# Kernel optimization log

Measured on AMD Instinct MI355X. Metric: run time of the kernel, lower is better.

The kernel has to match this reference:

```python
import jax, jax.numpy as jnp
import numpy as np

BLOCK_SIZE = 64
NUM_STEPS = 3
# pad_type='post', init_type='ones', attention_mask=None


def setup_inputs() -> dict:
    key = jax.random.key(0)
    k1, k2, k3 = jax.random.split(key, 3)
    B, H, S, D = 4, 16, 4096, 64
    return {
        "query": jax.random.normal(k1, (B, H, S, D), dtype=jnp.float32),
        "key": jax.random.normal(k2, (B, H, S, D), dtype=jnp.float32),
        "value": jax.random.normal(k3, (B, H, S, D), dtype=jnp.float32),
    }


def _soba_monarch(query, key, value):
    B, H, S, D = query.shape
    bs = BLOCK_SIZE
    nb = -(-S // bs)                 # ceil(S / bs)
    pad = nb * bs - S                # post padding amount
    q = query / (D ** 0.5)

    pad_cfg = ((0, 0), (0, 0), (0, pad), (0, 0))
    Qb = jnp.pad(q, pad_cfg).reshape(B, H, nb, bs, D)      # (l j) v -> l j v
    Kb = jnp.pad(key, pad_cfg).reshape(B, H, nb, bs, D)    # (k i) v -> k i v

    # validity of positions in the padded sequence (post-pad)
    pos_valid = (jnp.arange(nb * bs) < S).reshape(nb, bs)  # [block, within]
    # left factor shape (..., j, l, k): rows of the flattened (l j) axis
    left_mask = jnp.broadcast_to(pos_valid.T[:, :, None], (bs, nb, nb))      # j l k
    # right factor shape (..., k, j, i): columns of the flattened (k i) axis
    right_mask = jnp.broadcast_to(pos_valid[:, None, :], (nb, bs, bs))       # k j i

    NEG = jnp.finfo(q.dtype).min
    # init_type = 'ones'
    left = jnp.broadcast_to(
        jnp.where(left_mask, 1.0 / nb, 0.0), (B, H, bs, nb, nb)
    ).astype(q.dtype)

    for _ in range(NUM_STEPS):
        # beta[k,j,i] = sum_{l,v} left[j,l,k] Q[l,j,v] K[k,i,v]
        beta = jnp.einsum('bhjlk,bhljv,bhkiv->bhkji', left, Qb, Kb, optimize=True)
        tau = jnp.swapaxes(jnp.sum(left, axis=-2), -1, -2)[..., None]        # bhkj1
        tau_zero = jnp.isclose(tau, 0.0)
        tau_safe = jnp.where(tau_zero, 1.0, tau)
        logits_r = jnp.where(right_mask & ~tau_zero, beta / tau_safe, NEG)
        right = jax.nn.softmax(logits_r, axis=-1)
        right = jnp.where(right_mask, right, 0.0)

        # alpha[j,1,k] = sum_i right[k,j,i] log right[k,j,i]  (xlogy)
        r_safe = jnp.where(right > 0, right, 1.0)
        alpha = jnp.sum(right * jnp.log(r_safe), axis=-1)                    # bhkj
        alpha = jnp.swapaxes(alpha, -1, -2)[..., None, :]                    # bhj1k

        beta2 = jnp.einsum('bhkji,bhljv,bhkiv->bhjlk', right, Qb, Kb, optimize=True)
        left = jax.nn.softmax(jnp.where(left_mask, beta2 - alpha, NEG), axis=-1)
        left = jnp.where(left_mask, left, 0.0)

    # multiply: z = L (R V)
    Vb = jnp.pad(value, pad_cfg).reshape(B, H, nb, bs, D)                    # k i v
    Y = jnp.einsum('bhkji,bhkiv->bhkjv', right, Vb)
    Z = jnp.einsum('bhjlk,bhkjv->bhljv', left, Y)
    z = Z.reshape(B, H, nb * bs, D)
    return z[..., :S, :]


def reference(query, key, value):
    return _soba_monarch(query, key, value)
```

## Files before the change

kernel.cpp:

```cpp
#include <hip/hip_runtime.h>


namespace {

typedef __attribute__((ext_vector_type(8))) short short8v;
typedef __attribute__((ext_vector_type(4))) float f32x4;

constexpr int HEADS = 64;
constexpr size_t HEADQ = 262144;
constexpr size_t MATF  = (size_t)HEADS * 262144;

#define MFMA(ACC, A, B) ACC = __builtin_amdgcn_mfma_f32_16x16x32_bf16(A, B, ACC, 0, 0, 0)
#define LD8(arr, row, g8) (*(const short8v*)((arr) + (row) * 72 + (g8) * 8))

__device__ __forceinline__ void bfsplit(float x, ushort& h, ushort& l) {
    uint u = __float_as_uint(x);
    uint hi = (u + 0x7FFFu + ((u >> 16) & 1u)) & 0xFFFF0000u;
    h = (ushort)(hi >> 16);
    l = (ushort)(__float_as_uint(x - __uint_as_float(hi)) >> 16);
}
__device__ __forceinline__ uint packbf(float x) {
    uint u = __float_as_uint(x);
    uint hi = (u + 0x7FFFu + ((u >> 16) & 1u)) & 0xFFFF0000u;
    return hi | (__float_as_uint(x - __uint_as_float(hi)) >> 16);
}

struct Frag16 { short8v h0, h1, l0, l1; };

__device__ __forceinline__ Frag16 split_load(const float* __restrict__ p, float s) {
    Frag16 f;
    #pragma unroll
    for (int q = 0; q < 4; ++q) {
        float4 a = *(const float4*)(p + 4 * q);
        float v[4] = {a.x * s, a.y * s, a.z * s, a.w * s};
        #pragma unroll
        for (int e = 0; e < 4; ++e) {
            ushort hh, ll; bfsplit(v[e], hh, ll);
            const int i = 4 * q + e;
            if (i < 8) { f.h0[i] = (short)hh; f.l0[i] = (short)ll; }
            else       { f.h1[i - 8] = (short)hh; f.l1[i - 8] = (short)ll; }
        }
    }
    return f;
}
__device__ __forceinline__ Frag16 unpack_load(const uint* __restrict__ p) {
    Frag16 f;
    #pragma unroll
    for (int q = 0; q < 2; ++q) {
        uint4 a = *(const uint4*)(p + 8 * q);
        uint4 b = *(const uint4*)(p + 8 * q + 4);
        uint vv[8] = {a.x, a.y, a.z, a.w, b.x, b.y, b.z, b.w};
        short8v h, l;
        #pragma unroll
        for (int e = 0; e < 8; ++e) {
            h[e] = (short)(vv[e] >> 16);
            l[e] = (short)(vv[e] & 0xFFFFu);
        }
        if (q == 0) { f.h0 = h; f.l0 = l; } else { f.h1 = h; f.l1 = l; }
    }
    return f;
}
__device__ __forceinline__ void store_rows(ushort* H, ushort* L, int r, int c0,
                                           const Frag16& f) {
    *(short8v*)(H + r * 72 + c0)     = f.h0;
    *(short8v*)(H + r * 72 + c0 + 8) = f.h1;
    *(short8v*)(L + r * 72 + c0)     = f.l0;
    *(short8v*)(L + r * 72 + c0 + 8) = f.l1;
}
__device__ __forceinline__ void scatter_tr(ushort* H, ushort* L, int r, int c0,
                                           const Frag16& f) {
    #pragma unroll
    for (int e = 0; e < 8; ++e) {
        H[(c0 + e) * 72 + r] = (ushort)f.h0[e];
        L[(c0 + e) * 72 + r] = (ushort)f.l0[e];
    }
    #pragma unroll
    for (int e = 0; e < 8; ++e) {
        H[(c0 + 8 + e) * 72 + r] = (ushort)f.h1[e];
        L[(c0 + 8 + e) * 72 + r] = (ushort)f.l1[e];
    }
}

__device__ __forceinline__ void mmstep(const ushort* AH, const ushort* AL,
                                       const ushort* BH, const ushort* BL,
                                       int w, int lo4, int hi4, f32x4 acc[4]) {
    #pragma unroll
    for (int ks = 0; ks < 2; ++ks) {
        short8v ah = LD8(AH, 16 * w + lo4, hi4 + 4 * ks);
        short8v al = LD8(AL, 16 * w + lo4, hi4 + 4 * ks);
        #pragma unroll
        for (int t = 0; t < 4; ++t) {
            short8v bh = LD8(BH, 16 * t + lo4, hi4 + 4 * ks);
            short8v bl = LD8(BL, 16 * t + lo4, hi4 + 4 * ks);
            MFMA(acc[t], ah, bh); MFMA(acc[t], ah, bl); MFMA(acc[t], al, bh);
        }
    }
}
__device__ __forceinline__ void mmstep_swap(const ushort* AH, const ushort* AL,
                                            const ushort* BH, const ushort* BL,
                                            int w, int lo4, int hi4, f32x4 acc[4]) {
    #pragma unroll
    for (int ks = 0; ks < 2; ++ks) {
        short8v bh = LD8(AH, 16 * w + lo4, hi4 + 4 * ks);
        short8v bl = LD8(AL, 16 * w + lo4, hi4 + 4 * ks);
        #pragma unroll
        for (int m = 0; m < 4; ++m) {
            short8v ah = LD8(BH, 16 * m + lo4, hi4 + 4 * ks);
            short8v al = LD8(BL, 16 * m + lo4, hi4 + 4 * ks);
            MFMA(acc[m], ah, bh); MFMA(acc[m], ah, bl); MFMA(acc[m], al, bh);
        }
    }
}

__device__ __forceinline__ float max16(const float* x) {
    float a = fmaxf(fmaxf(x[0], x[1]), fmaxf(x[2], x[3]));
    float b = fmaxf(fmaxf(x[4], x[5]), fmaxf(x[6], x[7]));
    float c = fmaxf(fmaxf(x[8], x[9]), fmaxf(x[10], x[11]));
    float d = fmaxf(fmaxf(x[12], x[13]), fmaxf(x[14], x[15]));
    return fmaxf(fmaxf(a, b), fmaxf(c, d));
}
__device__ __forceinline__ float sum16(const float* x) {
    float a = (x[0] + x[1]) + (x[2] + x[3]);
    float b = (x[4] + x[5]) + (x[6] + x[7]);
    float c = (x[8] + x[9]) + (x[10] + x[11]);
    float d = (x[12] + x[13]) + (x[14] + x[15]);
    return (a + b) + (c + d);
}

__global__ __launch_bounds__(256) void kmean_kernel(const float* __restrict__ Q,
                                                    uint* __restrict__ M) {
    const int wg = blockIdx.x;
    const int h  = wg >> 4;
    const int j  = ((wg & 15) << 2) + (threadIdx.x >> 6);
    const int v  = threadIdx.x & 63;
    const float* base = Q + (size_t)h * HEADQ + (size_t)j * 64 + v;
    float acc = 0.f;
    #pragma unroll
    for (int l = 0; l < 64; ++l) acc += base[(size_t)l * 4096];
    M[((size_t)h * 64 + j) * 64 + v] = packbf(acc * (1.0f / 512.0f));
}

template<int FIRST, int LAST>
__global__ __launch_bounds__(256, 4) void bc_kernel(
    const uint*  __restrict__ Gsrc,
    const float* __restrict__ Kmat,
    const float* __restrict__ Vmat,
    const float* __restrict__ tauIn,
    uint*  __restrict__ HmOut,
    float* __restrict__ alphaOut,
    uint*  __restrict__ Yout)
{
    __shared__ __align__(16) ushort SM[18432];
    ushort* Ah = SM;          ushort* Al = SM + 4608;
    ushort* Bh = SM + 9216;   ushort* Bl = SM + 13824;

    const int wg = blockIdx.x, h = wg >> 6, k = wg & 63;
    const int tid = threadIdx.x, r = tid & 63, c0 = (tid >> 6) << 4;
    const int w = tid >> 6, lo4 = tid & 15, hi4 = (tid >> 4) & 3;

    {
        const uint* gp = FIRST ? Gsrc + ((size_t)h * 64 + r) * 64 + c0
                               : Gsrc + ((size_t)h * 64 + r) * 4096 + (size_t)k * 64 + c0;
        store_rows(Ah, Al, r, c0, unpack_load(gp));
    }
    Frag16 fk = split_load(Kmat + (size_t)h * HEADQ + (size_t)k * 4096 + r * 64 + c0, 1.f);
    store_rows(Bh, Bl, r, c0, fk);
    Frag16 fv;
    if (LAST)
        fv = split_load(Vmat + (size_t)h * HEADQ + (size_t)k * 4096 + r * 64 + c0, 1.f);
    float tv = 1.f;
    if (!FIRST) tv = tauIn[((size_t)h * 64 + k) * 64 + 16 * w + lo4];
    __syncthreads();

    f32x4 acc[4] = {};
    mmstep_swap(Ah, Al, Bh, Bl, w, lo4, hi4, acc);
    __syncthreads();

    {
        const int j = 16 * w + lo4;
        const bool tz = !(tv > 1e-8f);
        const float tvi = tz ? 1.f : 1.f / tv;
        float x[16];
        #pragma unroll
        for (int m = 0; m < 4; ++m)
            #pragma unroll
            for (int rg = 0; rg < 4; ++rg) x[4 * m + rg] = acc[m][rg] * tvi;
        float mx = max16(x);
        mx = fmaxf(mx, __shfl_xor(mx, 16));
        mx = fmaxf(mx, __shfl_xor(mx, 32));
        #pragma unroll
        for (int e = 0; e < 16; ++e) x[e] = __expf(x[e] - mx);
        float s = sum16(x);
        s += __shfl_xor(s, 16);
        s += __shfl_xor(s, 32);
        const float inv = 1.f / s;
        float ap = 0.f;
        #pragma unroll
        for (int m = 0; m < 4; ++m) {
            #pragma unroll
            for (int rg = 0; rg < 4; ++rg) {
                const float rv = tz ? (1.f / 64.f) : x[4 * m + rg] * inv;
                ap += (rv > 0.f) ? rv * __logf(rv) : 0.f;
                ushort hh, ll; bfsplit(rv, hh, ll);
                const int i = 16 * m + 4 * hi4 + rg;
                Ah[j * 72 + i] = hh;
                Al[j * 72 + i] = ll;
            }
        }
        ap += __shfl_xor(ap, 16);
        ap += __shfl_xor(ap, 32);
        if (hi4 == 0) alphaOut[((size_t)h * 64 + j) * 64 + k] = ap;
    }
    scatter_tr(Bh, Bl, r, c0, fk);
    __syncthreads();

    f32x4 acc2[4] = {};
    mmstep(Ah, Al, Bh, Bl, w, lo4, hi4, acc2);
    #pragma unroll
    for (int rr = 0; rr < 4; ++rr) {
        const int j = 16 * w + 4 * hi4 + rr;
        const size_t ob = ((size_t)h * 64 + k) * 4096 + (size_t)j * 64;
        #pragma unroll
        for (int t = 0; t < 4; ++t)
            HmOut[ob + 16 * t + lo4] = packbf(acc2[t][rr]);
    }
    if (LAST) {
        __syncthreads();
        scatter_tr(Bh, Bl, r, c0, fv);
        __syncthreads();
        f32x4 acc3[4] = {};
        mmstep(Ah, Al, Bh, Bl, w, lo4, hi4, acc3);
        #pragma unroll
        for (int rr = 0; rr < 4; ++rr) {
            const int j = 16 * w + 4 * hi4 + rr;
            const size_t ob = ((size_t)h * 64 + k) * 4096 + (size_t)j * 64;
            #pragma unroll
            for (int t = 0; t < 4; ++t)
                Yout[ob + 16 * t + lo4] = packbf(acc3[t][rr]);
        }
    }
}

template<int LAST>
__global__ __launch_bounds__(256, 4) void da_kernel(
    const float* __restrict__ Q,
    const uint*  __restrict__ HmIn,
    const float* __restrict__ alphaIn,
    const uint*  __restrict__ Yin,
    uint*  __restrict__ Gout,
    float* __restrict__ tauOut,
    float* __restrict__ Zout)
{
    __shared__ __align__(16) ushort SM[18432];
    ushort* Ah = SM;          ushort* Al = SM + 4608;
    ushort* Bh = SM + 9216;   ushort* Bl = SM + 13824;

    const int wg = blockIdx.x, h = wg >> 6, j = wg & 63;
    const int tid = threadIdx.x, r = tid & 63, c0 = (tid >> 6) << 4;
    const int w = tid >> 6, lo4 = tid & 15, hi4 = (tid >> 4) & 3;

    Frag16 fq = split_load(Q + (size_t)h * HEADQ + (size_t)r * 4096 + (size_t)j * 64 + c0,
                           0.125f);
    store_rows(Ah, Al, r, c0, fq);
    {
        store_rows(Bh, Bl, r, c0,
                   unpack_load(HmIn + ((size_t)h * 64 + r) * 4096 + (size_t)j * 64 + c0));
    }
    Frag16 fy;
    if (LAST)
        fy = unpack_load(Yin + ((size_t)h * 64 + r) * 4096 + (size_t)j * 64 + c0);
    float av[16];
    {
        const float* ap0 = alphaIn + ((size_t)h * 64 + j) * 64 + 4 * hi4;
        #pragma unroll
        for (int m = 0; m < 4; ++m)
            #pragma unroll
            for (int rg = 0; rg < 4; ++rg) av[4 * m + rg] = ap0[16 * m + rg];
    }
    __syncthreads();

    f32x4 acc[4] = {};
    mmstep_swap(Ah, Al, Bh, Bl, w, lo4, hi4, acc);
    __syncthreads();

    {
        const int l = 16 * w + lo4;
        float x[16];
        #pragma unroll
        for (int m = 0; m < 4; ++m)
            #pragma unroll
            for (int rg = 0; rg < 4; ++rg) x[4 * m + rg] = acc[m][rg] - av[4 * m + rg];
        float mx = max16(x);
        mx = fmaxf(mx, __shfl_xor(mx, 16));
        mx = fmaxf(mx, __shfl_xor(mx, 32));
        #pragma unroll
        for (int e = 0; e < 16; ++e) x[e] = __expf(x[e] - mx);
        float s = sum16(x);
        s += __shfl_xor(s, 16);
        s += __shfl_xor(s, 32);
        const float inv = 1.f / s;
        #pragma unroll
        for (int m = 0; m < 4; ++m) {
            #pragma unroll
            for (int rg = 0; rg < 4; ++rg) {
                const float lv = x[4 * m + rg] * inv;
                ushort hh, ll; bfsplit(lv, hh, ll);
                const int kk = 16 * m + 4 * hi4 + rg;
                if (!LAST) { Bh[kk * 72 + l] = hh; Bl[kk * 72 + l] = ll; }
                else       { Bh[l * 72 + kk] = hh; Bl[l * 72 + kk] = ll; }
            }
        }
    }
    if (!LAST) scatter_tr(Ah, Al, r, c0, fq);
    else       scatter_tr(Ah, Al, r, c0, fy);
    __syncthreads();

    if (!LAST) {
        f32x4 acc2[4] = {};
        f32x4 tacc = {};
        short8v onesb;
        #pragma unroll
        for (int e2 = 0; e2 < 8; ++e2) onesb[e2] = (lo4 == 0) ? (short)0x3F80 : (short)0;
        #pragma unroll
        for (int ks = 0; ks < 2; ++ks) {
            short8v ah = LD8(Bh, 16 * w + lo4, hi4 + 4 * ks);
            short8v al = LD8(Bl, 16 * w + lo4, hi4 + 4 * ks);
            MFMA(tacc, ah, onesb); MFMA(tacc, al, onesb);
            #pragma unroll
            for (int t = 0; t < 4; ++t) {
                short8v bh = LD8(Ah, 16 * t + lo4, hi4 + 4 * ks);
                short8v bl = LD8(Al, 16 * t + lo4, hi4 + 4 * ks);
                MFMA(acc2[t], ah, bh); MFMA(acc2[t], ah, bl); MFMA(acc2[t], al, bh);
            }
        }
        #pragma unroll
        for (int rr = 0; rr < 4; ++rr) {
            const int kq = 16 * w + 4 * hi4 + rr;
            if (lo4 == 0) tauOut[((size_t)h * 64 + kq) * 64 + j] = tacc[rr];
            const size_t gb = ((size_t)h * 64 + j) * 4096 + (size_t)kq * 64;
            #pragma unroll
            for (int t = 0; t < 4; ++t) Gout[gb + 16 * t + lo4] = packbf(acc2[t][rr]);
        }
    } else {
        f32x4 acc2[4] = {};
        #pragma unroll
        for (int ks = 0; ks < 2; ++ks) {
            short8v ah = LD8(Bh, 16 * w + lo4, hi4 + 4 * ks);
            short8v al = LD8(Bl, 16 * w + lo4, hi4 + 4 * ks);
            #pragma unroll
            for (int t = 0; t < 4; ++t) {
                short8v bh = LD8(Ah, 16 * t + lo4, hi4 + 4 * ks);
                short8v bl = LD8(Al, 16 * t + lo4, hi4 + 4 * ks);
                MFMA(acc2[t], ah, bh); MFMA(acc2[t], ah, bl); MFMA(acc2[t], al, bh);
            }
        }
        #pragma unroll
        for (int rr = 0; rr < 4; ++rr) {
            const int l = 16 * w + 4 * hi4 + rr;
            const size_t zb = (size_t)h * HEADQ + (size_t)l * 4096 + (size_t)j * 64;
            #pragma unroll
            for (int t = 0; t < 4; ++t) Zout[zb + 16 * t + lo4] = acc2[t][rr];
        }
    }
}

}

extern "C" void kernel_launch(void* const* d_in, const int* in_sizes, int n_in,
                              void* d_out, int out_size, void* d_ws, size_t ws_size,
                              hipStream_t stream) {
    const float* Q = (const float*)d_in[0];
    const float* K = (const float*)d_in[1];
    const float* V = (const float*)d_in[2];
    float* out = (float*)d_out;

    char* ws = (char*)d_ws;
    const size_t MB = 1024 * 1024;
    uint*  G   = (uint*)(ws);
    uint*  Hm  = (uint*)(ws + 64 * MB);
    uint*  M   = (uint*)(ws + 128 * MB);
    float* al  = (float*)(ws + 129 * MB);
    float* tau = (float*)(ws + 130 * MB);

    const bool bigws = ws_size >= (size_t)195 * MB;
    uint*  Ybuf = bigws ? (uint*)(ws + 131 * MB) : (uint*)out;
    float* Zdst = bigws ? out : (float*)G;

    dim3 blk(256), grid(HEADS * 64);

    kmean_kernel<<<dim3(1024), blk, 0, stream>>>(Q, M);
    bc_kernel<1, 0><<<grid, blk, 0, stream>>>(M, K, nullptr, nullptr, Hm, al, nullptr);
    da_kernel<0>   <<<grid, blk, 0, stream>>>(Q, Hm, al, nullptr, G, tau, nullptr);
    bc_kernel<0, 0><<<grid, blk, 0, stream>>>(G, K, nullptr, tau, Hm, al, nullptr);
    da_kernel<0>   <<<grid, blk, 0, stream>>>(Q, Hm, al, nullptr, G, tau, nullptr);
    bc_kernel<0, 1><<<grid, blk, 0, stream>>>(G, K, V, tau, Hm, al, Ybuf);
    da_kernel<1>   <<<grid, blk, 0, stream>>>(Q, Hm, al, Ybuf, nullptr, nullptr, Zdst);
    if (!bigws)
        hipMemcpyAsync(d_out, Zdst, MATF * sizeof(float), hipMemcpyDeviceToDevice, stream);
}
```

Baseline: 310.6 us.

## Stage outputs through LDS for coalesced stores, swizzle workgroups, transpose tau/alpha layout

Output tiles (Hm, Y, G, Z) are first written to a padded LDS buffer and then flushed with 128-bit coalesced global stores, replacing scattered 4-byte stores. Workgroup IDs are remapped with an 8-way swizzle, which changes which blocks run close together and so may affect cache locality. The tau and alpha index layouts are transposed so their reads and writes follow the access pattern of the consuming kernel. The bf16 hi/lo split now uses the library conversion intrinsic. The LDS staging adds extra barriers and LDS traffic.

```diff
diff --git a/kernel.cpp b/kernel.cpp
--- a/kernel.cpp
+++ b/kernel.cpp
@@ -1,4 +1,5 @@
 #include <hip/hip_runtime.h>
+#include <hip/hip_bf16.h>
 
 
 namespace {
@@ -13,16 +14,19 @@
 #define MFMA(ACC, A, B) ACC = __builtin_amdgcn_mfma_f32_16x16x32_bf16(A, B, ACC, 0, 0, 0)
 #define LD8(arr, row, g8) (*(const short8v*)((arr) + (row) * 72 + (g8) * 8))
 
+__device__ __forceinline__ ushort bfh(float x) {
+    return __builtin_bit_cast(ushort, __float2bfloat16(x));
+}
+__device__ __forceinline__ float bf2f(ushort h) {
+    return __uint_as_float(((uint)h) << 16);
+}
 __device__ __forceinline__ void bfsplit(float x, ushort& h, ushort& l) {
-    uint u = __float_as_uint(x);
-    uint hi = (u + 0x7FFFu + ((u >> 16) & 1u)) & 0xFFFF0000u;
-    h = (ushort)(hi >> 16);
-    l = (ushort)(__float_as_uint(x - __uint_as_float(hi)) >> 16);
+    h = bfh(x);
+    l = bfh(x - bf2f(h));
 }
 __device__ __forceinline__ uint packbf(float x) {
-    uint u = __float_as_uint(x);
-    uint hi = (u + 0x7FFFu + ((u >> 16) & 1u)) & 0xFFFF0000u;
-    return hi | (__float_as_uint(x - __uint_as_float(hi)) >> 16);
+    ushort h, l; bfsplit(x, h, l);
+    return ((uint)h << 16) | l;
 }
 
 struct Frag16 { short8v h0, h1, l0, l1; };
@@ -81,6 +85,15 @@
     }
 }
 
+__device__ __forceinline__ void flush_u32(const uint* OS, uint* g, int tid) {
+    #pragma unroll
+    for (int q = 0; q < 4; ++q) {
+        const int off = tid * 4 + q * 1024;
+        uint4 v = *(const uint4*)(OS + (off >> 6) * 68 + (off & 63));
+        *(uint4*)(g + off) = v;
+    }
+}
+
 __device__ __forceinline__ void mmstep(const ushort* AH, const ushort* AL,
                                        const ushort* BH, const ushort* BL,
                                        int w, int lo4, int hi4, f32x4 acc[4]) {
@@ -127,9 +140,13 @@
     return (a + b) + (c + d);
 }
 
+__device__ __forceinline__ int swz_wg(int bid, int chunk) {
+    return (bid & 7) * chunk + (bid >> 3);
+}
+
 __global__ __launch_bounds__(256) void kmean_kernel(const float* __restrict__ Q,
                                                     uint* __restrict__ M) {
-    const int wg = blockIdx.x;
+    const int wg = swz_wg(blockIdx.x, 128);
     const int h  = wg >> 4;
     const int j  = ((wg & 15) << 2) + (threadIdx.x >> 6);
     const int v  = threadIdx.x & 63;
@@ -153,8 +170,10 @@
     __shared__ __align__(16) ushort SM[18432];
     ushort* Ah = SM;          ushort* Al = SM + 4608;
     ushort* Bh = SM + 9216;   ushort* Bl = SM + 13824;
-
-    const int wg = blockIdx.x, h = wg >> 6, k = wg & 63;
+    uint* OSA = (uint*)SM;
+    uint* OSB = (uint*)(SM + 9216);
+
+    const int wg = swz_wg(blockIdx.x, 512), h = wg >> 6, k = wg & 63;
     const int tid = threadIdx.x, r = tid & 63, c0 = (tid >> 6) << 4;
     const int w = tid >> 6, lo4 = tid & 15, hi4 = (tid >> 4) & 3;
 
@@ -169,7 +188,7 @@
     if (LAST)
         fv = split_load(Vmat + (size_t)h * HEADQ + (size_t)k * 4096 + r * 64 + c0, 1.f);
     float tv = 1.f;
-    if (!FIRST) tv = tauIn[((size_t)h * 64 + k) * 64 + 16 * w + lo4];
+    if (!FIRST) tv = tauIn[((size_t)h * 64 + 16 * w + lo4) * 64 + k];
     __syncthreads();
 
     f32x4 acc[4] = {};
@@ -209,35 +228,44 @@
         }
         ap += __shfl_xor(ap, 16);
         ap += __shfl_xor(ap, 32);
-        if (hi4 == 0) alphaOut[((size_t)h * 64 + j) * 64 + k] = ap;
+        if (hi4 == 0) alphaOut[((size_t)h * 64 + k) * 64 + j] = ap;
     }
     scatter_tr(Bh, Bl, r, c0, fk);
     __syncthreads();
 
     f32x4 acc2[4] = {};
     mmstep(Ah, Al, Bh, Bl, w, lo4, hi4, acc2);
-    #pragma unroll
-    for (int rr = 0; rr < 4; ++rr) {
-        const int j = 16 * w + 4 * hi4 + rr;
-        const size_t ob = ((size_t)h * 64 + k) * 4096 + (size_t)j * 64;
-        #pragma unroll
-        for (int t = 0; t < 4; ++t)
-            HmOut[ob + 16 * t + lo4] = packbf(acc2[t][rr]);
-    }
-    if (LAST) {
+    const size_t ob = ((size_t)h * 64 + k) * 4096;
+    if (!LAST) {
+        __syncthreads();
+        #pragma unroll
+        for (int rr = 0; rr < 4; ++rr) {
+            const int j = 16 * w + 4 * hi4 + rr;
+            #pragma unroll
+            for (int t = 0; t < 4; ++t)
+                OSB[j * 68 + 16 * t + lo4] = packbf(acc2[t][rr]);
+        }
+        __syncthreads();
+        flush_u32(OSB, HmOut + ob, tid);
+    } else {
         __syncthreads();
         scatter_tr(Bh, Bl, r, c0, fv);
         __syncthreads();
         f32x4 acc3[4] = {};
         mmstep(Ah, Al, Bh, Bl, w, lo4, hi4, acc3);
+        __syncthreads();
         #pragma unroll
         for (int rr = 0; rr < 4; ++rr) {
             const int j = 16 * w + 4 * hi4 + rr;
-            const size_t ob = ((size_t)h * 64 + k) * 4096 + (size_t)j * 64;
-            #pragma unroll
-            for (int t = 0; t < 4; ++t)
-                Yout[ob + 16 * t + lo4] = packbf(acc3[t][rr]);
-        }
+            #pragma unroll
+            for (int t = 0; t < 4; ++t) {
+                OSA[j * 68 + 16 * t + lo4] = packbf(acc2[t][rr]);
+                OSB[j * 68 + 16 * t + lo4] = packbf(acc3[t][rr]);
+            }
+        }
+        __syncthreads();
+        flush_u32(OSA, HmOut + ob, tid);
+        flush_u32(OSB, Yout + ob, tid);
     }
 }
 
@@ -254,8 +282,10 @@
     __shared__ __align__(16) ushort SM[18432];
     ushort* Ah = SM;          ushort* Al = SM + 4608;
     ushort* Bh = SM + 9216;   ushort* Bl = SM + 13824;
-
-    const int wg = blockIdx.x, h = wg >> 6, j = wg & 63;
+    uint*  OSB = (uint*)(SM + 9216);
+    float* OSF = (float*)(SM + 9216);
+
+    const int wg = swz_wg(blockIdx.x, 512), h = wg >> 6, j = wg & 63;
     const int tid = threadIdx.x, r = tid & 63, c0 = (tid >> 6) << 4;
     const int w = tid >> 6, lo4 = tid & 15, hi4 = (tid >> 4) & 3;
 
@@ -270,13 +300,11 @@
     if (LAST)
         fy = unpack_load(Yin + ((size_t)h * 64 + r) * 4096 + (size_t)j * 64 + c0);
     float av[16];
-    {
-        const float* ap0 = alphaIn + ((size_t)h * 64 + j) * 64 + 4 * hi4;
-        #pragma unroll
-        for (int m = 0; m < 4; ++m)
-            #pragma unroll
-            for (int rg = 0; rg < 4; ++rg) av[4 * m + rg] = ap0[16 * m + rg];
-    }
+    #pragma unroll
+    for (int m = 0; m < 4; ++m)
+        #pragma unroll
+        for (int rg = 0; rg < 4; ++rg)
+            av[4 * m + rg] = alphaIn[((size_t)h * 64 + 16 * m + 4 * hi4 + rg) * 64 + j];
     __syncthreads();
 
     f32x4 acc[4] = {};
@@ -333,14 +361,17 @@
                 MFMA(acc2[t], ah, bh); MFMA(acc2[t], ah, bl); MFMA(acc2[t], al, bh);
             }
         }
+        __syncthreads();
         #pragma unroll
         for (int rr = 0; rr < 4; ++rr) {
             const int kq = 16 * w + 4 * hi4 + rr;
-            if (lo4 == 0) tauOut[((size_t)h * 64 + kq) * 64 + j] = tacc[rr];
-            const size_t gb = ((size_t)h * 64 + j) * 4096 + (size_t)kq * 64;
-            #pragma unroll
-            for (int t = 0; t < 4; ++t) Gout[gb + 16 * t + lo4] = packbf(acc2[t][rr]);
-        }
+            if (lo4 == 0) tauOut[((size_t)h * 64 + j) * 64 + kq] = tacc[rr];
+            #pragma unroll
+            for (int t = 0; t < 4; ++t)
+                OSB[kq * 68 + 16 * t + lo4] = packbf(acc2[t][rr]);
+        }
+        __syncthreads();
+        flush_u32(OSB, Gout + ((size_t)h * 64 + j) * 4096, tid);
     } else {
         f32x4 acc2[4] = {};
         #pragma unroll
@@ -354,12 +385,20 @@
                 MFMA(acc2[t], ah, bh); MFMA(acc2[t], ah, bl); MFMA(acc2[t], al, bh);
             }
         }
+        __syncthreads();
         #pragma unroll
         for (int rr = 0; rr < 4; ++rr) {
             const int l = 16 * w + 4 * hi4 + rr;
-            const size_t zb = (size_t)h * HEADQ + (size_t)l * 4096 + (size_t)j * 64;
-            #pragma unroll
-            for (int t = 0; t < 4; ++t) Zout[zb + 16 * t + lo4] = acc2[t][rr];
+            #pragma unroll
+            for (int t = 0; t < 4; ++t) OSF[l * 68 + 16 * t + lo4] = acc2[t][rr];
+        }
+        __syncthreads();
+        #pragma unroll
+        for (int q = 0; q < 4; ++q) {
+            const int l = (tid >> 4) + 16 * q;
+            const int v4 = (tid & 15) * 4;
+            float4 vv = *(const float4*)(OSF + l * 68 + v4);
+            *(float4*)(Zout + (size_t)h * HEADQ + (size_t)l * 4096 + (size_t)j * 64 + v4) = vv;
         }
     }
 }
```

Result: slower. 334.9 us (+7.8%).

## Store intermediates as fp32 and stage outputs through LDS for coalesced writes

Applied to the files above, without the earlier changes.

Intermediate matrices (G, Hm, Y, M) are now stored as plain fp32 instead of packed bf16 hi/lo pairs, and the consumer re-splits them on load. All outputs are first staged in shared memory with a padded stride, then written to global memory as contiguous float4 stores instead of scattered scalar stores from MFMA accumulator layout. The aim is better-coalesced global writes and less pack/unpack arithmetic. It costs extra LDS round-trips and barriers, plus re-splitting on the load side. Since a packed uint and a float are the same size, memory traffic stays about the same.

```diff
diff --git a/kernel.cpp b/kernel.cpp
--- a/kernel.cpp
+++ b/kernel.cpp
@@ -19,11 +19,6 @@
     h = (ushort)(hi >> 16);
     l = (ushort)(__float_as_uint(x - __uint_as_float(hi)) >> 16);
 }
-__device__ __forceinline__ uint packbf(float x) {
-    uint u = __float_as_uint(x);
-    uint hi = (u + 0x7FFFu + ((u >> 16) & 1u)) & 0xFFFF0000u;
-    return hi | (__float_as_uint(x - __uint_as_float(hi)) >> 16);
-}
 
 struct Frag16 { short8v h0, h1, l0, l1; };
 
@@ -40,23 +35,6 @@
             if (i < 8) { f.h0[i] = (short)hh; f.l0[i] = (short)ll; }
             else       { f.h1[i - 8] = (short)hh; f.l1[i - 8] = (short)ll; }
         }
-    }
-    return f;
-}
-__device__ __forceinline__ Frag16 unpack_load(const uint* __restrict__ p) {
-    Frag16 f;
-    #pragma unroll
-    for (int q = 0; q < 2; ++q) {
-        uint4 a = *(const uint4*)(p + 8 * q);
-        uint4 b = *(const uint4*)(p + 8 * q + 4);
-        uint vv[8] = {a.x, a.y, a.z, a.w, b.x, b.y, b.z, b.w};
-        short8v h, l;
-        #pragma unroll
-        for (int e = 0; e < 8; ++e) {
-            h[e] = (short)(vv[e] >> 16);
-            l[e] = (short)(vv[e] & 0xFFFFu);
-        }
-        if (q == 0) { f.h0 = h; f.l0 = l; } else { f.h1 = h; f.l1 = l; }
     }
     return f;
 }
@@ -81,6 +59,15 @@
     }
 }
 
+__device__ __forceinline__ void flush_f32(const float* OS, float* g, int tid) {
+    #pragma unroll
+    for (int q = 0; q < 4; ++q) {
+        const int off = tid * 4 + q * 1024;
+        float4 v = *(const float4*)(OS + (off >> 6) * 68 + (off & 63));
+        *(float4*)(g + off) = v;
+    }
+}
+
 __device__ __forceinline__ void mmstep(const ushort* AH, const ushort* AL,
                                        const ushort* BH, const ushort* BL,
                                        int w, int lo4, int hi4, f32x4 acc[4]) {
@@ -128,7 +115,7 @@
 }
 
 __global__ __launch_bounds__(256) void kmean_kernel(const float* __restrict__ Q,
-                                                    uint* __restrict__ M) {
+                                                    float* __restrict__ M) {
     const int wg = blockIdx.x;
     const int h  = wg >> 4;
     const int j  = ((wg & 15) << 2) + (threadIdx.x >> 6);
@@ -137,31 +124,33 @@
     float acc = 0.f;
     #pragma unroll
     for (int l = 0; l < 64; ++l) acc += base[(size_t)l * 4096];
-    M[((size_t)h * 64 + j) * 64 + v] = packbf(acc * (1.0f / 512.0f));
+    M[((size_t)h * 64 + j) * 64 + v] = acc * (1.0f / 512.0f);
 }
 
 template<int FIRST, int LAST>
 __global__ __launch_bounds__(256, 4) void bc_kernel(
-    const uint*  __restrict__ Gsrc,
+    const float* __restrict__ Gsrc,
     const float* __restrict__ Kmat,
     const float* __restrict__ Vmat,
     const float* __restrict__ tauIn,
-    uint*  __restrict__ HmOut,
+    float* __restrict__ HmOut,
     float* __restrict__ alphaOut,
-    uint*  __restrict__ Yout)
+    float* __restrict__ Yout)
 {
     __shared__ __align__(16) ushort SM[18432];
     ushort* Ah = SM;          ushort* Al = SM + 4608;
     ushort* Bh = SM + 9216;   ushort* Bl = SM + 13824;
+    float* OSA = (float*)SM;
+    float* OSB = (float*)(SM + 9216);
 
     const int wg = blockIdx.x, h = wg >> 6, k = wg & 63;
     const int tid = threadIdx.x, r = tid & 63, c0 = (tid >> 6) << 4;
     const int w = tid >> 6, lo4 = tid & 15, hi4 = (tid >> 4) & 3;
 
     {
-        const uint* gp = FIRST ? Gsrc + ((size_t)h * 64 + r) * 64 + c0
-                               : Gsrc + ((size_t)h * 64 + r) * 4096 + (size_t)k * 64 + c0;
-        store_rows(Ah, Al, r, c0, unpack_load(gp));
+        const float* gp = FIRST ? Gsrc + ((size_t)h * 64 + r) * 64 + c0
+                                : Gsrc + ((size_t)h * 64 + r) * 4096 + (size_t)k * 64 + c0;
+        store_rows(Ah, Al, r, c0, split_load(gp, 1.f));
     }
     Frag16 fk = split_load(Kmat + (size_t)h * HEADQ + (size_t)k * 4096 + r * 64 + c0, 1.f);
     store_rows(Bh, Bl, r, c0, fk);
@@ -216,44 +205,54 @@
 
     f32x4 acc2[4] = {};
     mmstep(Ah, Al, Bh, Bl, w, lo4, hi4, acc2);
-    #pragma unroll
-    for (int rr = 0; rr < 4; ++rr) {
-        const int j = 16 * w + 4 * hi4 + rr;
-        const size_t ob = ((size_t)h * 64 + k) * 4096 + (size_t)j * 64;
-        #pragma unroll
-        for (int t = 0; t < 4; ++t)
-            HmOut[ob + 16 * t + lo4] = packbf(acc2[t][rr]);
-    }
-    if (LAST) {
+    const size_t ob = ((size_t)h * 64 + k) * 4096;
+    if (!LAST) {
+        __syncthreads();
+        #pragma unroll
+        for (int rr = 0; rr < 4; ++rr) {
+            const int j = 16 * w + 4 * hi4 + rr;
+            #pragma unroll
+            for (int t = 0; t < 4; ++t)
+                OSB[j * 68 + 16 * t + lo4] = acc2[t][rr];
+        }
+        __syncthreads();
+        flush_f32(OSB, HmOut + ob, tid);
+    } else {
         __syncthreads();
         scatter_tr(Bh, Bl, r, c0, fv);
         __syncthreads();
         f32x4 acc3[4] = {};
         mmstep(Ah, Al, Bh, Bl, w, lo4, hi4, acc3);
+        __syncthreads();
         #pragma unroll
         for (int rr = 0; rr < 4; ++rr) {
             const int j = 16 * w + 4 * hi4 + rr;
-            const size_t ob = ((size_t)h * 64 + k) * 4096 + (size_t)j * 64;
-            #pragma unroll
-            for (int t = 0; t < 4; ++t)
-                Yout[ob + 16 * t + lo4] = packbf(acc3[t][rr]);
-        }
+            #pragma unroll
+            for (int t = 0; t < 4; ++t) {
+                OSA[j * 68 + 16 * t + lo4] = acc2[t][rr];
+                OSB[j * 68 + 16 * t + lo4] = acc3[t][rr];
+            }
+        }
+        __syncthreads();
+        flush_f32(OSA, HmOut + ob, tid);
+        flush_f32(OSB, Yout + ob, tid);
     }
 }
 
 template<int LAST>
 __global__ __launch_bounds__(256, 4) void da_kernel(
     const float* __restrict__ Q,
-    const uint*  __restrict__ HmIn,
+    const float* __restrict__ HmIn,
     const float* __restrict__ alphaIn,
-    const uint*  __restrict__ Yin,
-    uint*  __restrict__ Gout,
+    const float* __restrict__ Yin,
+    float* __restrict__ Gout,
     float* __restrict__ tauOut,
     float* __restrict__ Zout)
 {
     __shared__ __align__(16) ushort SM[18432];
     ushort* Ah = SM;          ushort* Al = SM + 4608;
     ushort* Bh = SM + 9216;   ushort* Bl = SM + 13824;
+    float* OSB = (float*)(SM + 9216);
 
     const int wg = blockIdx.x, h = wg >> 6, j = wg & 63;
     const int tid = threadIdx.x, r = tid & 63, c0 = (tid >> 6) << 4;
@@ -264,11 +263,11 @@
     store_rows(Ah, Al, r, c0, fq);
     {
         store_rows(Bh, Bl, r, c0,
-                   unpack_load(HmIn + ((size_t)h * 64 + r) * 4096 + (size_t)j * 64 + c0));
+                   split_load(HmIn + ((size_t)h * 64 + r) * 4096 + (size_t)j * 64 + c0, 1.f));
     }
     Frag16 fy;
     if (LAST)
-        fy = unpack_load(Yin + ((size_t)h * 64 + r) * 4096 + (size_t)j * 64 + c0);
+        fy = split_load(Yin + ((size_t)h * 64 + r) * 4096 + (size_t)j * 64 + c0, 1.f);
     float av[16];
     {
         const float* ap0 = alphaIn + ((size_t)h * 64 + j) * 64 + 4 * hi4;
@@ -333,14 +332,17 @@
                 MFMA(acc2[t], ah, bh); MFMA(acc2[t], ah, bl); MFMA(acc2[t], al, bh);
             }
         }
+        __syncthreads();
         #pragma unroll
         for (int rr = 0; rr < 4; ++rr) {
             const int kq = 16 * w + 4 * hi4 + rr;
             if (lo4 == 0) tauOut[((size_t)h * 64 + kq) * 64 + j] = tacc[rr];
-            const size_t gb = ((size_t)h * 64 + j) * 4096 + (size_t)kq * 64;
-            #pragma unroll
-            for (int t = 0; t < 4; ++t) Gout[gb + 16 * t + lo4] = packbf(acc2[t][rr]);
-        }
+            #pragma unroll
+            for (int t = 0; t < 4; ++t)
+                OSB[kq * 68 + 16 * t + lo4] = acc2[t][rr];
+        }
+        __syncthreads();
+        flush_f32(OSB, Gout + ((size_t)h * 64 + j) * 4096, tid);
     } else {
         f32x4 acc2[4] = {};
         #pragma unroll
@@ -354,12 +356,20 @@
                 MFMA(acc2[t], ah, bh); MFMA(acc2[t], ah, bl); MFMA(acc2[t], al, bh);
             }
         }
+        __syncthreads();
         #pragma unroll
         for (int rr = 0; rr < 4; ++rr) {
             const int l = 16 * w + 4 * hi4 + rr;
-            const size_t zb = (size_t)h * HEADQ + (size_t)l * 4096 + (size_t)j * 64;
-            #pragma unroll
-            for (int t = 0; t < 4; ++t) Zout[zb + 16 * t + lo4] = acc2[t][rr];
+            #pragma unroll
+            for (int t = 0; t < 4; ++t) OSB[l * 68 + 16 * t + lo4] = acc2[t][rr];
+        }
+        __syncthreads();
+        #pragma unroll
+        for (int q = 0; q < 4; ++q) {
+            const int l = (tid >> 4) + 16 * q;
+            const int v4 = (tid & 15) * 4;
+            float4 vv = *(const float4*)(OSB + l * 68 + v4);
+            *(float4*)(Zout + (size_t)h * HEADQ + (size_t)l * 4096 + (size_t)j * 64 + v4) = vv;
         }
     }
 }
@@ -376,15 +386,15 @@
 
     char* ws = (char*)d_ws;
     const size_t MB = 1024 * 1024;
-    uint*  G   = (uint*)(ws);
-    uint*  Hm  = (uint*)(ws + 64 * MB);
-    uint*  M   = (uint*)(ws + 128 * MB);
+    float* G   = (float*)(ws);
+    float* Hm  = (float*)(ws + 64 * MB);
+    float* M   = (float*)(ws + 128 * MB);
     float* al  = (float*)(ws + 129 * MB);
     float* tau = (float*)(ws + 130 * MB);
 
     const bool bigws = ws_size >= (size_t)195 * MB;
-    uint*  Ybuf = bigws ? (uint*)(ws + 131 * MB) : (uint*)out;
-    float* Zdst = bigws ? out : (float*)G;
+    float* Ybuf = bigws ? (float*)(ws + 131 * MB) : out;
+    float* Zdst = bigws ? out : G;
 
     dim3 blk(256), grid(HEADS * 64);
 
```

Result: no change. 305.4 us (-1.7%).
